# Optimization experiments

Hardware: AMD Instinct MI355X
Metric: run time of the kernel (lower is better)

Reference implementation:

```python
import jax, jax.numpy as jnp
import numpy as np

B, T, I, H, O = 64, 512, 128, 1024, 128
FORGET_BIAS = 1.0  # TF LSTMCell default


def setup_inputs() -> dict:
    key = jax.random.key(0)
    k1, k2, k3 = jax.random.split(key, 3)
    X = jax.random.normal(k1, (B, T, I), dtype=jnp.float32)
    Wk = jax.random.normal(k2, (I + H, 4 * H), dtype=jnp.float32) * 0.02
    b = jnp.zeros((4 * H,), dtype=jnp.float32)
    Wd = jax.random.normal(k3, (H, O), dtype=jnp.float32) * 0.02
    bd = jnp.zeros((O,), dtype=jnp.float32)
    return {"X": X, "Wk": Wk, "b": b, "Wd": Wd, "bd": bd}


def _lstm(X, Wk, b):
    # TF LSTMCell with activation=relu; gate order in kernel: i, j, f, o
    batch = X.shape[0]
    h = X.shape[-1]  # not used; keep shapes explicit below
    c0 = jnp.zeros((batch, H), dtype=X.dtype)
    h0 = jnp.zeros((batch, H), dtype=X.dtype)

    def step(carry, x_t):
        c, hs = carry
        z = jnp.concatenate([x_t, hs], axis=-1) @ Wk + b  # [B, 4H]
        i, j, f, o = jnp.split(z, 4, axis=-1)
        i = jax.nn.sigmoid(i)
        f = jax.nn.sigmoid(f + FORGET_BIAS)
        o = jax.nn.sigmoid(o)
        g = jax.nn.relu(j)          # cell-input activation (custom relu)
        c_new = f * c + i * g
        h_new = o * jax.nn.relu(c_new)  # output activation (custom relu)
        return (c_new, h_new), h_new

    xs = jnp.swapaxes(X, 0, 1)  # [T, B, I]
    _, hs = jax.lax.scan(step, (c0, h0), xs)
    return jnp.swapaxes(hs, 0, 1)  # [B, T, H]


def reference(X, Wk, b, Wd, bd):
    rnn_out = _lstm(X, Wk, b)          # [B, T, H]
    outputs = rnn_out @ Wd + bd        # [B, T, O] (SL=True: dense per timestep)
    return outputs
```

## Files before the change

### kernel.cpp

```cpp
#include <hip/hip_runtime.h>
#include <math.h>

#define Bsz 64
#define Tn  512
#define In  128
#define Hn  1024
#define KT  1152
#define NBLK 128

typedef __attribute__((ext_vector_type(8))) short bf16x8;
typedef __attribute__((ext_vector_type(4))) short s16x4;
typedef __attribute__((ext_vector_type(4))) float f32x4;
typedef __attribute__((ext_vector_type(4))) int   i32x4;

__device__ void llvm_amdgcn_raw_buffer_store_i16(short vdata, i32x4 srsrc, int voffset, int soffset, int cpol) __asm("llvm.amdgcn.raw.buffer.store.i16");
__device__ i32x4 llvm_amdgcn_raw_buffer_load_v4i32(i32x4 srsrc, int voffset, int soffset, int cpol) __asm("llvm.amdgcn.raw.buffer.load.v4i32");

__device__ __forceinline__ i32x4 make_srd(const void* p, int bytes) {
  i32x4 r;
  r.x = (int)(unsigned)(unsigned long long)p;
  r.y = (int)((unsigned long long)p >> 32);
  r.z = bytes;
  r.w = 0x00020000;
  return r;
}

__device__ __forceinline__ bf16x8 as_bf16x8(i32x4 v) {
  union { i32x4 i; bf16x8 b; } u; u.i = v; return u.b;
}

__device__ __forceinline__ unsigned short f2bf(float f) {
  union { float f; unsigned u; } x; x.f = f;
  unsigned r = x.u + 0x7FFFu + ((x.u >> 16) & 1u);
  return (unsigned short)(r >> 16);
}
__device__ __forceinline__ float sigmoidf_(float x) { return 1.0f / (1.0f + __expf(-x)); }

__global__ __launch_bounds__(256) void cast_x_kernel(const float* __restrict__ in,
                                                     unsigned short* __restrict__ out) {
  int i = blockIdx.x * 256 + threadIdx.x;
  f32x4 v = ((const f32x4*)in)[i];
  s16x4 o;
  o.x = (short)f2bf(v.x); o.y = (short)f2bf(v.y);
  o.z = (short)f2bf(v.z); o.w = (short)f2bf(v.w);
  ((s16x4*)out)[i] = o;
}

__global__ __launch_bounds__(256) void transpose_cast_kernel(const float* __restrict__ in,
                                                             unsigned short* __restrict__ out,
                                                             int R, int C, int ldo, int tilesR) {
  __shared__ unsigned short tile[64][73];
  int br = blockIdx.x % tilesR, bc = blockIdx.x / tilesR;
  int r0 = br << 6, c0 = bc << 6;
  for (int e = threadIdx.x; e < 4096; e += 256) {
    int r = e >> 6, c = e & 63;
    tile[r][c] = f2bf(in[(size_t)(r0 + r) * C + (c0 + c)]);
  }
  __syncthreads();
  for (int e = threadIdx.x; e < 4096; e += 256) {
    int c = e >> 6, r = e & 63;
    out[(size_t)(c0 + c) * ldo + (r0 + r)] = tile[r][c];
  }
}

__global__ __launch_bounds__(512, 1) void lstm_kernel(
    const unsigned short* __restrict__ Xb,
    const unsigned short* __restrict__ WkT,
    const float* __restrict__ bias,
    unsigned short* __restrict__ hs,
    unsigned* __restrict__ S)
{
  __shared__ float Z4[4][64][36];
  const int tid = threadIdx.x;
  const int blk = blockIdx.x;
  const int w   = tid >> 6;
  const int mh  = w & 1;
  const int kq  = w >> 1;
  const int l   = tid & 63, q = l >> 4, n16 = l & 15;

  const i32x4 hsrd = make_srd(hs, Tn * Bsz * Hn * 2);

  bf16x8 Bf[2][9];
#pragma unroll
  for (int nt = 0; nt < 2; ++nt) {
    int cl   = nt * 16 + n16;
    int gcol = (cl >> 3) * Hn + blk * 8 + (cl & 7);
    const unsigned short* bp = WkT + (size_t)gcol * KT;
    Bf[nt][0] = *(const bf16x8*)(bp + kq * 32 + q * 8);
#pragma unroll
    for (int ks = 1; ks < 9; ++ks)
      Bf[nt][ks] = *(const bf16x8*)(bp + 128 + kq * 256 + (ks - 1) * 32 + q * 8);
  }

  const int eb = tid >> 3, ej = tid & 7;
  const float bi  = bias[           blk * 8 + ej];
  const float bg  = bias[    Hn   + blk * 8 + ej];
  const float bfg = bias[2 * Hn   + blk * 8 + ej] + 1.0f;
  const float bo  = bias[3 * Hn   + blk * 8 + ej];
  const int   hst_off = (eb * Hn + blk * 8 + ej) * 2;
  float cst = 0.0f;

  const int b0 = mh * 32 + n16;
  const int b1 = b0 + 16;
  const int ho0 = (b0 * Hn + kq * 256 + q * 8) * 2;
  const int ho1 = (b1 * Hn + kq * 256 + q * 8) * 2;

  for (int t = 0; t < Tn; ++t) {
    f32x4 a00 = {0,0,0,0}, a01 = {0,0,0,0}, a10 = {0,0,0,0}, a11 = {0,0,0,0};

    bf16x8 X0 = *(const bf16x8*)(Xb + ((size_t)b0 * Tn + t) * In + kq * 32 + q * 8);
    bf16x8 X1 = *(const bf16x8*)(Xb + ((size_t)b1 * Tn + t) * In + kq * 32 + q * 8);
    a00 = __builtin_amdgcn_mfma_f32_16x16x32_bf16(X0, Bf[0][0], a00, 0, 0, 0);
    a01 = __builtin_amdgcn_mfma_f32_16x16x32_bf16(X0, Bf[1][0], a01, 0, 0, 0);
    a10 = __builtin_amdgcn_mfma_f32_16x16x32_bf16(X1, Bf[0][0], a10, 0, 0, 0);
    a11 = __builtin_amdgcn_mfma_f32_16x16x32_bf16(X1, Bf[1][0], a11, 0, 0, 0);

    if (t > 0) {
      const int tb = (t - 1) * (Bsz * Hn * 2);
      i32x4 H0[8], H1[8];
      for (;;) {
        asm volatile("" ::: "memory");
#pragma unroll
        for (int ks = 0; ks < 8; ++ks) {
          H0[ks] = llvm_amdgcn_raw_buffer_load_v4i32(hsrd, tb + ho0 + ks * 64, 0, 17);
          H1[ks] = llvm_amdgcn_raw_buffer_load_v4i32(hsrd, tb + ho1 + ks * 64, 0, 17);
        }
        int bad = 0;
#pragma unroll
        for (int ks = 0; ks < 8; ++ks) {
          bad |= H0[ks].x | H0[ks].y | H0[ks].z | H0[ks].w;
          bad |= H1[ks].x | H1[ks].y | H1[ks].z | H1[ks].w;
        }
        if (__ballot(((unsigned)bad & 0x80008000u) == 0u) == ~0ull) break;
        __builtin_amdgcn_s_sleep(1);
      }
#pragma unroll
      for (int ks = 0; ks < 8; ++ks) {
        bf16x8 A0 = as_bf16x8(H0[ks]);
        bf16x8 A1 = as_bf16x8(H1[ks]);
        a00 = __builtin_amdgcn_mfma_f32_16x16x32_bf16(A0, Bf[0][ks + 1], a00, 0, 0, 0);
        a01 = __builtin_amdgcn_mfma_f32_16x16x32_bf16(A0, Bf[1][ks + 1], a01, 0, 0, 0);
        a10 = __builtin_amdgcn_mfma_f32_16x16x32_bf16(A1, Bf[0][ks + 1], a10, 0, 0, 0);
        a11 = __builtin_amdgcn_mfma_f32_16x16x32_bf16(A1, Bf[1][ks + 1], a11, 0, 0, 0);
      }
    }

#pragma unroll
    for (int r = 0; r < 4; ++r) {
      int row = mh * 32 + q * 4 + r;
      Z4[kq][row     ][     n16] = a00[r];
      Z4[kq][row     ][16 + n16] = a01[r];
      Z4[kq][row + 16][     n16] = a10[r];
      Z4[kq][row + 16][16 + n16] = a11[r];
    }
    asm volatile("s_waitcnt lgkmcnt(0)" ::: "memory");
    __builtin_amdgcn_s_barrier();

    float zi = bi, zg = bg, zf = bfg, zo = bo;
#pragma unroll
    for (int k2 = 0; k2 < 4; ++k2) {
      zi += Z4[k2][eb][     ej];
      zg += Z4[k2][eb][ 8 + ej];
      zf += Z4[k2][eb][16 + ej];
      zo += Z4[k2][eb][24 + ej];
    }
    float ig = sigmoidf_(zi);
    float g  = fmaxf(zg, 0.0f);
    float ff = sigmoidf_(zf);
    float oo = sigmoidf_(zo);
    cst = ff * cst + ig * g;
    float hn = oo * fmaxf(cst, 0.0f);
    llvm_amdgcn_raw_buffer_store_i16((short)f2bf(hn), hsrd,
                                     t * (Bsz * Hn * 2) + hst_off, 0, 17);

    asm volatile("s_waitcnt lgkmcnt(0)" ::: "memory");
    __builtin_amdgcn_s_barrier();
  }
}

__global__ __launch_bounds__(256) void dense_kernel(
    const unsigned short* __restrict__ hs,
    const unsigned short* __restrict__ WdT,
    const float* __restrict__ bd,
    float* __restrict__ out)
{
  const int tid = threadIdx.x;
  const int w = tid >> 6, l = tid & 63, q = l >> 4, n16 = l & 15;
  const int R0 = blockIdx.x * 64 + w * 16;
  f32x4 acc[8];
#pragma unroll
  for (int i = 0; i < 8; ++i) acc[i] = (f32x4){0, 0, 0, 0};
  const unsigned short* arow = hs + (size_t)(R0 + n16) * Hn + q * 8;
#pragma unroll 4
  for (int ks = 0; ks < 32; ++ks) {
    bf16x8 A = *(const bf16x8*)(arow + ks * 32);
#pragma unroll
    for (int nt = 0; nt < 8; ++nt) {
      bf16x8 Bf = *(const bf16x8*)(WdT + (size_t)(nt * 16 + n16) * Hn + ks * 32 + q * 8);
      acc[nt] = __builtin_amdgcn_mfma_f32_16x16x32_bf16(A, Bf, acc[nt], 0, 0, 0);
    }
  }
#pragma unroll
  for (int nt = 0; nt < 8; ++nt) {
    int col = nt * 16 + n16;
    float bdv = bd[col];
#pragma unroll
    for (int r = 0; r < 4; ++r) {
      int R = R0 + q * 4 + r;
      int b = R & 63, t = R >> 6;
      out[((size_t)b * Tn + t) * 128 + col] = acc[nt][r] + bdv;
    }
  }
}

extern "C" void kernel_launch(void* const* d_in, const int* in_sizes, int n_in,
                              void* d_out, int out_size, void* d_ws, size_t ws_size,
                              hipStream_t stream) {
  const float* X    = (const float*)d_in[0];
  const float* Wk   = (const float*)d_in[1];
  const float* bias = (const float*)d_in[2];
  const float* Wd   = (const float*)d_in[3];
  const float* bd   = (const float*)d_in[4];
  float* out = (float*)d_out;

  char* ws = (char*)d_ws;
  unsigned short* Xb  = (unsigned short*)(ws);
  unsigned short* WkT = (unsigned short*)(ws + 8388608);
  unsigned short* WdT = (unsigned short*)(ws + 17825792);
  unsigned short* hs  = (unsigned short*)(ws + 18087936);
  unsigned*       syn = (unsigned*)      (ws + 85196800);

  hipMemsetAsync(hs, 0xFF, 67108864, stream);
  hipMemsetAsync(syn, 0, 4096, stream);
  cast_x_kernel<<<4096, 256, 0, stream>>>(X, Xb);
  transpose_cast_kernel<<<1152, 256, 0, stream>>>(Wk, WkT, 1152, 4096, 1152, 18);
  transpose_cast_kernel<<<32, 256, 0, stream>>>(Wd, WdT, 1024, 128, 1024, 16);
  lstm_kernel<<<NBLK, 512, 0, stream>>>(Xb, WkT, bias, hs, syn);
  dense_kernel<<<512, 256, 0, stream>>>(hs, WdT, bd, out);
}
```

Before: 3.068 ms.

## Replace sentinel polling of hidden states with per-wave step flag counters

```diff
diff --git a/kernel.cpp b/kernel.cpp
--- a/kernel.cpp
+++ b/kernel.cpp
@@ -14,6 +14,7 @@
 typedef __attribute__((ext_vector_type(4))) int   i32x4;
 
 __device__ void llvm_amdgcn_raw_buffer_store_i16(short vdata, i32x4 srsrc, int voffset, int soffset, int cpol) __asm("llvm.amdgcn.raw.buffer.store.i16");
+__device__ void llvm_amdgcn_raw_buffer_store_i32(int vdata, i32x4 srsrc, int voffset, int soffset, int cpol) __asm("llvm.amdgcn.raw.buffer.store.i32");
 __device__ i32x4 llvm_amdgcn_raw_buffer_load_v4i32(i32x4 srsrc, int voffset, int soffset, int cpol) __asm("llvm.amdgcn.raw.buffer.load.v4i32");
 
 __device__ __forceinline__ i32x4 make_srd(const void* p, int bytes) {
@@ -23,10 +24,6 @@
   r.z = bytes;
   r.w = 0x00020000;
   return r;
-}
-
-__device__ __forceinline__ bf16x8 as_bf16x8(i32x4 v) {
-  union { i32x4 i; bf16x8 b; } u; u.i = v; return u.b;
 }
 
 __device__ __forceinline__ unsigned short f2bf(float f) {
@@ -79,6 +76,7 @@
   const int l   = tid & 63, q = l >> 4, n16 = l & 15;
 
   const i32x4 hsrd = make_srd(hs, Tn * Bsz * Hn * 2);
+  const i32x4 ssrd = make_srd(S, 4096);
 
   bf16x8 Bf[2][9];
 #pragma unroll
@@ -102,8 +100,7 @@
 
   const int b0 = mh * 32 + n16;
   const int b1 = b0 + 16;
-  const int ho0 = (b0 * Hn + kq * 256 + q * 8) * 2;
-  const int ho1 = (b1 * Hn + kq * 256 + q * 8) * 2;
+  const int so = ((32 * kq + (l & 31)) * 8 + 4 * mh) * 4;
 
   for (int t = 0; t < Tn; ++t) {
     f32x4 a00 = {0,0,0,0}, a01 = {0,0,0,0}, a10 = {0,0,0,0}, a11 = {0,0,0,0};
@@ -116,28 +113,22 @@
     a11 = __builtin_amdgcn_mfma_f32_16x16x32_bf16(X1, Bf[1][0], a11, 0, 0, 0);
 
     if (t > 0) {
-      const int tb = (t - 1) * (Bsz * Hn * 2);
-      i32x4 H0[8], H1[8];
+      const unsigned tgt = (unsigned)t;
       for (;;) {
         asm volatile("" ::: "memory");
-#pragma unroll
-        for (int ks = 0; ks < 8; ++ks) {
-          H0[ks] = llvm_amdgcn_raw_buffer_load_v4i32(hsrd, tb + ho0 + ks * 64, 0, 17);
-          H1[ks] = llvm_amdgcn_raw_buffer_load_v4i32(hsrd, tb + ho1 + ks * 64, 0, 17);
-        }
-        int bad = 0;
-#pragma unroll
-        for (int ks = 0; ks < 8; ++ks) {
-          bad |= H0[ks].x | H0[ks].y | H0[ks].z | H0[ks].w;
-          bad |= H1[ks].x | H1[ks].y | H1[ks].z | H1[ks].w;
-        }
-        if (__ballot(((unsigned)bad & 0x80008000u) == 0u) == ~0ull) break;
+        i32x4 v = llvm_amdgcn_raw_buffer_load_v4i32(ssrd, so, 0, 17);
+        unsigned ma = (unsigned)v.x < (unsigned)v.y ? (unsigned)v.x : (unsigned)v.y;
+        unsigned mc = (unsigned)v.z < (unsigned)v.w ? (unsigned)v.z : (unsigned)v.w;
+        ma = ma < mc ? ma : mc;
+        if (__ballot(ma >= tgt) == ~0ull) break;
         __builtin_amdgcn_s_sleep(1);
       }
+      const unsigned short* hrow = hs + (size_t)(t - 1) * (Bsz * Hn);
 #pragma unroll
       for (int ks = 0; ks < 8; ++ks) {
-        bf16x8 A0 = as_bf16x8(H0[ks]);
-        bf16x8 A1 = as_bf16x8(H1[ks]);
+        int kh = kq * 256 + ks * 32 + q * 8;
+        bf16x8 A0 = *(const bf16x8*)(hrow + (size_t)b0 * Hn + kh);
+        bf16x8 A1 = *(const bf16x8*)(hrow + (size_t)b1 * Hn + kh);
         a00 = __builtin_amdgcn_mfma_f32_16x16x32_bf16(A0, Bf[0][ks + 1], a00, 0, 0, 0);
         a01 = __builtin_amdgcn_mfma_f32_16x16x32_bf16(A0, Bf[1][ks + 1], a01, 0, 0, 0);
         a10 = __builtin_amdgcn_mfma_f32_16x16x32_bf16(A1, Bf[0][ks + 1], a10, 0, 0, 0);
@@ -172,6 +163,10 @@
     float hn = oo * fmaxf(cst, 0.0f);
     llvm_amdgcn_raw_buffer_store_i16((short)f2bf(hn), hsrd,
                                      t * (Bsz * Hn * 2) + hst_off, 0, 17);
+
+    asm volatile("s_waitcnt vmcnt(0)" ::: "memory");
+    if (t < Tn - 1 && l == 0)
+      llvm_amdgcn_raw_buffer_store_i32((int)(t + 1), ssrd, (blk * 8 + w) * 4, 0, 17);
 
     asm volatile("s_waitcnt lgkmcnt(0)" ::: "memory");
     __builtin_amdgcn_s_barrier();
@@ -230,7 +225,6 @@
   unsigned short* hs  = (unsigned short*)(ws + 18087936);
   unsigned*       syn = (unsigned*)      (ws + 85196800);
 
-  hipMemsetAsync(hs, 0xFF, 67108864, stream);
   hipMemsetAsync(syn, 0, 4096, stream);
   cast_x_kernel<<<4096, 256, 0, stream>>>(X, Xb);
   transpose_cast_kernel<<<1152, 256, 0, stream>>>(Wk, WkT, 1152, 4096, 1152, 18);
```

New measurement: 2.961 ms. 1.04x faster.
